# Kernel tuning notes

Hardware: AMD Instinct MI355X
Metric: run time of the kernel (lower is better)

The kernel has to match this reference:

```python
import jax, jax.numpy as jnp
import numpy as np

N_MEMORY = 16
FEA_DIM = 512


def setup_inputs() -> dict:
    key = jax.random.key(0)
    ks = jax.random.split(key, 8)
    b, L, d, n = 4, 4096, FEA_DIM, N_MEMORY
    scale = 1.0 / np.sqrt(d)  # ~ torch Linear default init scale
    return {
        "query": jax.random.normal(ks[0], (b, L, d), dtype=jnp.float32),
        "W1": jax.random.uniform(ks[1], (n, d, d), jnp.float32, -scale, scale),
        "b1": jax.random.uniform(ks[2], (n, d), jnp.float32, -scale, scale),
        "W2": jax.random.uniform(ks[3], (n, d, d), jnp.float32, -scale, scale),
        "b2": jax.random.uniform(ks[4], (n, d), jnp.float32, -scale, scale),
        "Wg": jax.random.uniform(ks[5], (n, d), jnp.float32, -scale, scale),
        "bg": jax.random.uniform(ks[6], (n,), jnp.float32, -scale, scale),
        "topk": 8,
    }


def reference(query, W1, b1, W2, b2, Wg, bg, topk):
    # query: [b, L, d]; stacked per-memory-slot params: W1/W2 [n, d, d], Wg [n, d]
    n = W1.shape[0]
    # per-slot LeakyReLU negative slopes: 0.01 + 0.2/n * l
    slopes = (0.01 + 0.2 / n * jnp.arange(n, dtype=query.dtype))[:, None, None, None]
    # memory_function: Linear -> LeakyReLU(slope_l) -> Linear -> Tanh, all slots at once
    h = jnp.einsum('bld,ndh->nblh', query, W1) + b1[:, None, None, :]   # [n,b,L,d]
    h = jnp.where(h >= 0, h, h * slopes)
    x = jnp.tanh(jnp.einsum('nblh,nhd->nbld', h, W2) + b2[:, None, None, :])  # [n,b,L,d]
    # gate: Linear(d,1) -> softmax over L -> topk over L -> gather -> weighted sum
    logits = jnp.einsum('nbld,nd->nbl', x, Wg) + bg[:, None, None]      # [n,b,L]
    w = jax.nn.softmax(logits, axis=-1)
    top_w, top_idx = jax.lax.top_k(w, topk)                             # [n,b,k]
    items = jnp.take_along_axis(x, top_idx[..., None], axis=2)          # [n,b,k,d]
    combined = jnp.einsum('nbkd,nbk->nbd', items, top_w)                # [n,b,d]
    m_item = jnp.transpose(combined, (1, 0, 2))                         # [b,n,d]
    # F.normalize(dim=-1), eps=1e-12
    norm = jnp.maximum(jnp.linalg.norm(m_item, axis=-1, keepdims=True), 1e-12)
    return m_item / norm
```

## Files before the change

kernel.cpp:

```cpp
#include <hip/hip_runtime.h>
#include <hip/hip_bf16.h>
#include <cstdint>
#include <cstddef>

#define NMEM 16
#define DDIM 512
#define BATCH 4
#define LSEQ 4096
#define ROWS 16384
#define NCAND 32
#define KTOP 8
#define QPAD 20

typedef __attribute__((ext_vector_type(4))) float f32x4;
typedef __attribute__((ext_vector_type(16))) float f32x16;
typedef __attribute__((ext_vector_type(8))) int int8v;

__device__ inline void gld16(const void* gptr, void* lptr) {
    __builtin_amdgcn_global_load_lds(
        (const __attribute__((address_space(1))) unsigned int*)gptr,
        (__attribute__((address_space(3))) unsigned int*)lptr,
        16, 0, 0);
}

__device__ inline float fast_tanh(float x) {
    float t = __builtin_amdgcn_fmed3f(x, -3.f, 3.f);
    float t2 = t * t;
    return t * (27.f + t2) * __builtin_amdgcn_rcpf(27.f + 9.f * t2);
}

__device__ inline int8v ldg_frag(const unsigned char* p) {
    int4 x = *(const int4*)p;
    int4 y = *(const int4*)(p + 16);
    int8v v;
    v[0] = x.x; v[1] = x.y; v[2] = x.z; v[3] = x.w;
    v[4] = y.x; v[5] = y.y; v[6] = y.z; v[7] = y.w;
    return v;
}

__device__ inline int8v load_frag_half(const unsigned char* Ts, int row, int kh) {
    int key = (row >> 1) & 3;
    const int4* p0 = (const int4*)(Ts + row * 64 + ((((kh << 1) | 0) ^ key) << 4));
    const int4* p1 = (const int4*)(Ts + row * 64 + ((((kh << 1) | 1) ^ key) << 4));
    int4 x = *p0, y = *p1;
    int8v v;
    v[0] = x.x; v[1] = x.y; v[2] = x.z; v[3] = x.w;
    v[4] = y.x; v[5] = y.y; v[6] = y.z; v[7] = y.w;
    return v;
}

__device__ inline void stage_half(const unsigned char* Wbase, unsigned char* dst,
                                  int tid) {
    #pragma unroll
    for (int i = 0; i < 2; ++i) {
        int c = i * 256 + tid;
        int row = c >> 2, s = c & 3;
        gld16(Wbase + (size_t)row * DDIM + ((s ^ ((row >> 1) & 3)) << 4),
              dst + c * 16);
    }
}

__global__ __launch_bounds__(256)
void prep_kernel(const float* __restrict__ query,
                 const float* __restrict__ W1, const float* __restrict__ W2,
                 unsigned char* __restrict__ Q8,
                 unsigned char* __restrict__ W1T8, unsigned char* __restrict__ W2T8) {
    int blk = blockIdx.x, t = threadIdx.x;
    if (blk < 2048) {
        size_t base = ((size_t)blk * 256 + t) * 16;
        const float4* in = (const float4*)(query + base);
        int4 o; int* op = (int*)&o;
        #pragma unroll
        for (int q = 0; q < 4; ++q) {
            float4 v = in[q];
            int lo = __builtin_amdgcn_cvt_pk_fp8_f32(v.x, v.y, 0, false);
            op[q] = __builtin_amdgcn_cvt_pk_fp8_f32(v.z, v.w, lo, true);
        }
        *(int4*)(Q8 + base) = o;
    } else {
        __shared__ float tile[64][69];
        int bid = blk - 2048;
        const float* Win = W1; unsigned char* Wout = W1T8;
        if (bid >= 1024) { bid -= 1024; Win = W2; Wout = W2T8; }
        int n = bid >> 6, t64 = bid & 63;
        int dt = (t64 >> 3) << 6, jt = (t64 & 7) << 6;
        const float* inN = Win + (size_t)n * DDIM * DDIM;
        unsigned char* outN = Wout + (size_t)n * DDIM * DDIM;
        int rr = t >> 4, cc = (t & 15) * 4;
        #pragma unroll
        for (int pass = 0; pass < 4; ++pass) {
            int row = rr + pass * 16;
            float4 v = *(const float4*)(inN + (size_t)(dt + row) * DDIM + jt + cc);
            tile[row][cc] = v.x; tile[row][cc + 1] = v.y;
            tile[row][cc + 2] = v.z; tile[row][cc + 3] = v.w;
        }
        __syncthreads();
        #pragma unroll
        for (int pass = 0; pass < 4; ++pass) {
            int jl = rr + pass * 16;
            float f0 = tile[cc][jl], f1 = tile[cc + 1][jl];
            float f2 = tile[cc + 2][jl], f3 = tile[cc + 3][jl];
            int lo = __builtin_amdgcn_cvt_pk_fp8_f32(f0, f1, 0, false);
            int dw = __builtin_amdgcn_cvt_pk_fp8_f32(f2, f3, lo, true);
            *(int*)(outN + (size_t)(jt + jl) * DDIM + dt + cc) = dw;
        }
    }
}

__global__ __launch_bounds__(256, 4)
void fused_mlp_kernel(const unsigned char* __restrict__ Q8,
                      const unsigned char* __restrict__ W1T8,
                      const unsigned char* __restrict__ W2T8,
                      const float* __restrict__ b1, const float* __restrict__ b2,
                      const float* __restrict__ Wg,
                      float* __restrict__ logits)
{
    __shared__ unsigned char hbuf[32 * 512];
    __shared__ unsigned char Bs[2][8192];
    __shared__ float lsum[4][32];
    const int id = blockIdx.x;
    const int n = id & 15;
    const int m0 = (id >> 4) * 32;
    const int tid = threadIdx.x, lane = tid & 63;
    const int w = tid >> 6;
    const int l31 = lane & 31, kh = lane >> 5;
    const unsigned char* W1n = W1T8 + (size_t)n * DDIM * DDIM;
    const unsigned char* W2n = W2T8 + (size_t)n * DDIM * DDIM;
    const float slope = 0.01f + 0.0125f * n;
    const unsigned char* Aq0 = Q8 + (size_t)(m0 + l31) * DDIM + kh * 32;

    int8v avq[8];
    #pragma unroll
    for (int qa = 0; qa < 8; ++qa)
        avq[qa] = ldg_frag(Aq0 + qa * 64);
    stage_half(W1n, Bs[0], tid);
    __syncthreads();

    #pragma unroll 1
    for (int n0 = 0; n0 < 4; ++n0) {
        f32x16 acc = {};
        #pragma unroll
        for (int p8 = 0; p8 < 8; ++p8) {
            const int P = n0 * 8 + p8, Pn = P + 1;
            const unsigned char* nsrc = (Pn < 32)
                ? W1n + (size_t)((Pn >> 3) * 128) * DDIM + (Pn & 7) * 64
                : W2n;
            stage_half(nsrc, Bs[Pn & 1], tid);
            const unsigned char* Ts = Bs[P & 1];
            int8v wfr = load_frag_half(Ts, w * 32 + l31, kh);
            acc = __builtin_amdgcn_mfma_scale_f32_32x32x64_f8f6f4(
                wfr, avq[p8], acc, 0, 0, 0, 0x7F7F7F7F, 0, 0x7F7F7F7F);
            __syncthreads();
        }
        {
            int r = l31;
            #pragma unroll
            for (int q = 0; q < 4; ++q) {
                int jb = n0 * 128 + w * 32 + 8 * q + 4 * kh;
                float4 bias = *(const float4*)(b1 + n * DDIM + jb);
                float v0 = acc[4 * q + 0] + bias.x;
                float v1 = acc[4 * q + 1] + bias.y;
                float v2 = acc[4 * q + 2] + bias.z;
                float v3 = acc[4 * q + 3] + bias.w;
                v0 = v0 >= 0.f ? v0 : v0 * slope;
                v1 = v1 >= 0.f ? v1 : v1 * slope;
                v2 = v2 >= 0.f ? v2 : v2 * slope;
                v3 = v3 >= 0.f ? v3 : v3 * slope;
                int lo = __builtin_amdgcn_cvt_pk_fp8_f32(v0, v1, 0, false);
                int dw = __builtin_amdgcn_cvt_pk_fp8_f32(v2, v3, lo, true);
                *(int*)(hbuf + r * 512 + ((((jb >> 4) ^ (r & 7)) << 4) | (jb & 15))) = dw;
            }
        }
    }

    __syncthreads();

    float rowacc[16] = {};
    #pragma unroll 1
    for (int n0 = 0; n0 < 4; ++n0) {
        f32x16 acc = {};
        #pragma unroll 1
        for (int p8 = 0; p8 < 8; ++p8) {
            const int P = 32 + n0 * 8 + p8, Pn = P + 1;
            if (Pn < 64)
                stage_half(W2n + (size_t)(((Pn - 32) >> 3) * 128) * DDIM
                               + ((Pn - 32) & 7) * 64,
                           Bs[Pn & 1], tid);
            int hrow = l31, hq = hrow & 7;
            int C0 = p8 * 4 + 2 * kh;
            int8v hv;
            {
                const int4* p0 = (const int4*)(hbuf + hrow * 512 + ((C0 ^ hq) << 4));
                const int4* p1 = (const int4*)(hbuf + hrow * 512 + (((C0 + 1) ^ hq) << 4));
                int4 x = *p0, y = *p1;
                hv[0] = x.x; hv[1] = x.y; hv[2] = x.z; hv[3] = x.w;
                hv[4] = y.x; hv[5] = y.y; hv[6] = y.z; hv[7] = y.w;
            }
            const unsigned char* Ts = Bs[P & 1];
            int8v wfr = load_frag_half(Ts, w * 32 + l31, kh);
            acc = __builtin_amdgcn_mfma_scale_f32_32x32x64_f8f6f4(
                hv, wfr, acc, 0, 0, 0, 0x7F7F7F7F, 0, 0x7F7F7F7F);
            __syncthreads();
        }
        {
            int j = n0 * 128 + w * 32 + l31;
            float bias = b2[n * DDIM + j];
            float wgv = Wg[n * DDIM + j];
            #pragma unroll
            for (int reg = 0; reg < 16; ++reg)
                rowacc[reg] = fmaf(fast_tanh(acc[reg] + bias), wgv, rowacc[reg]);
        }
    }
    #pragma unroll
    for (int sh = 1; sh < 32; sh <<= 1)
        #pragma unroll
        for (int reg = 0; reg < 16; ++reg)
            rowacc[reg] += __shfl_xor(rowacc[reg], sh);
    if (l31 == 0) {
        #pragma unroll
        for (int reg = 0; reg < 16; ++reg)
            lsum[w][(reg & 3) + 8 * (reg >> 2) + 4 * kh] = rowacc[reg];
    }
    __syncthreads();
    if (tid < 32)
        logits[(size_t)n * ROWS + m0 + tid] =
            lsum[0][tid] + lsum[1][tid] + lsum[2][tid] + lsum[3][tid];
}

__global__ __launch_bounds__(256)
void topcand_kernel(const float* __restrict__ logits, int* __restrict__ cand,
                    float* __restrict__ ex_logit) {
    __shared__ float lv[LSEQ];
    __shared__ float cv[128];
    __shared__ int   ci[128];
    int p = blockIdx.x, n = p >> 2, b = p & 3;
    int t = threadIdx.x, lane = t & 63, w = t >> 6;
    const float* L = logits + (size_t)n * ROWS + (size_t)b * LSEQ;
    for (int i = t; i < LSEQ; i += 256) lv[i] = L[i];
    __syncthreads();
    float mv[16];
    int base = w * 1024;
    #pragma unroll
    for (int j = 0; j < 16; ++j) mv[j] = lv[base + j * 64 + lane];
    for (int rd = 0; rd < 32; ++rd) {
        float best = mv[0]; int bj = 0;
        #pragma unroll
        for (int j = 1; j < 16; ++j)
            if (mv[j] > best) { best = mv[j]; bj = j; }
        int bidx = base + bj * 64 + lane;
        float rv = best; int ridx = bidx;
        #pragma unroll
        for (int s = 1; s < 64; s <<= 1) {
            float ov = __shfl_xor(rv, s); int oi = __shfl_xor(ridx, s);
            if (ov > rv || (ov == rv && oi < ridx)) { rv = ov; ridx = oi; }
        }
        if (lane == 0) { cv[w * 32 + rd] = rv; ci[w * 32 + rd] = ridx; }
        if (ridx == bidx) mv[bj] = -1e30f;
    }
    __syncthreads();
    if (w == 0) {
        float v2[2]; int i2[2];
        #pragma unroll
        for (int k = 0; k < 2; ++k) { v2[k] = cv[k * 64 + lane]; i2[k] = ci[k * 64 + lane]; }
        for (int rd = 0; rd < 32; ++rd) {
            float best = v2[0]; int bi = i2[0]; int bk = 0;
            if (v2[1] > best || (v2[1] == best && i2[1] < bi)) { best = v2[1]; bi = i2[1]; bk = 1; }
            float rv = best; int ridx = bi;
            #pragma unroll
            for (int s = 1; s < 64; s <<= 1) {
                float ov = __shfl_xor(rv, s); int oi = __shfl_xor(ridx, s);
                if (ov > rv || (ov == rv && oi < ridx)) { rv = ov; ridx = oi; }
            }
            if (lane == 0) cand[p * NCAND + rd] = ridx;
            if (ridx == bi) v2[bk] = -1e30f;
        }
    } else if (w == 1) {
        if (lane < NCAND) ex_logit[p * NCAND + lane] = 0.f;
    }
}

__global__ __launch_bounds__(256)
void exact_h_kernel(const float* __restrict__ query,
                    const float* __restrict__ W1, const float* __restrict__ b1,
                    const int* __restrict__ cand, float* __restrict__ ex_h) {
    __shared__ float qs[DDIM][QPAD];
    __shared__ float hpart[4][16][64];
    int blk = blockIdx.x;
    int p = blk >> 4, r4 = blk & 15;
    int ct = r4 >> 3, jc = r4 & 7;
    int n = p >> 2, b = p & 3;
    int t = threadIdx.x, jj = t & 63, dg = t >> 6;
    int j = jc * 64 + jj;
    for (int c = 0; c < 16; ++c) {
        int li = cand[p * NCAND + ct * 16 + c];
        const float* qr = query + ((size_t)b * LSEQ + li) * DDIM;
        for (int d = t; d < DDIM; d += 256) qs[d][c] = qr[d];
    }
    __syncthreads();
    const float* W1n = W1 + (size_t)n * DDIM * DDIM;
    float acc[16] = {};
    for (int d = dg * 128; d < dg * 128 + 128; ++d) {
        float wvv = W1n[(size_t)d * DDIM + j];
        const float4* qv = (const float4*)&qs[d][0];
        #pragma unroll
        for (int c4 = 0; c4 < 4; ++c4) {
            float4 q4 = qv[c4];
            acc[c4 * 4 + 0] = fmaf(q4.x, wvv, acc[c4 * 4 + 0]);
            acc[c4 * 4 + 1] = fmaf(q4.y, wvv, acc[c4 * 4 + 1]);
            acc[c4 * 4 + 2] = fmaf(q4.z, wvv, acc[c4 * 4 + 2]);
            acc[c4 * 4 + 3] = fmaf(q4.w, wvv, acc[c4 * 4 + 3]);
        }
    }
    #pragma unroll
    for (int c = 0; c < 16; ++c) hpart[dg][c][jj] = acc[c];
    __syncthreads();
    const float slope = 0.01f + 0.0125f * n;
    float bias = b1[n * DDIM + j];
    for (int cc = dg; cc < 16; cc += 4) {
        float h = hpart[0][cc][jj] + hpart[1][cc][jj] + hpart[2][cc][jj]
                + hpart[3][cc][jj] + bias;
        h = h >= 0.f ? h : h * slope;
        ex_h[((size_t)p * NCAND + ct * 16 + cc) * DDIM + j] = h;
    }
}

__global__ __launch_bounds__(256)
void exact_x_kernel(const float* __restrict__ ex_h,
                    const float* __restrict__ W2, const float* __restrict__ b2,
                    const float* __restrict__ Wg,
                    float* __restrict__ ex_x, float* __restrict__ ex_logit) {
    __shared__ float hs[DDIM][QPAD];
    __shared__ float xpart[4][16][64];
    int blk = blockIdx.x;
    int p = blk >> 4, r4 = blk & 15;
    int ct = r4 >> 3, jc = r4 & 7;
    int n = p >> 2;
    int t = threadIdx.x, jj = t & 63, dg = t >> 6;
    int j = jc * 64 + jj;
    for (int c = 0; c < 16; ++c) {
        const float* hr = ex_h + ((size_t)p * NCAND + ct * 16 + c) * DDIM;
        for (int d = t; d < DDIM; d += 256) hs[d][c] = hr[d];
    }
    __syncthreads();
    const float* W2n = W2 + (size_t)n * DDIM * DDIM;
    float acc[16] = {};
    for (int d = dg * 128; d < dg * 128 + 128; ++d) {
        float wvv = W2n[(size_t)d * DDIM + j];
        const float4* hv = (const float4*)&hs[d][0];
        #pragma unroll
        for (int c4 = 0; c4 < 4; ++c4) {
            float4 h4 = hv[c4];
            acc[c4 * 4 + 0] = fmaf(h4.x, wvv, acc[c4 * 4 + 0]);
            acc[c4 * 4 + 1] = fmaf(h4.y, wvv, acc[c4 * 4 + 1]);
            acc[c4 * 4 + 2] = fmaf(h4.z, wvv, acc[c4 * 4 + 2]);
            acc[c4 * 4 + 3] = fmaf(h4.w, wvv, acc[c4 * 4 + 3]);
        }
    }
    #pragma unroll
    for (int c = 0; c < 16; ++c) xpart[dg][c][jj] = acc[c];
    __syncthreads();
    float bias = b2[n * DDIM + j];
    float wg = Wg[n * DDIM + j];
    for (int cc = dg; cc < 16; cc += 4) {
        float a = xpart[0][cc][jj] + xpart[1][cc][jj] + xpart[2][cc][jj]
                + xpart[3][cc][jj] + bias;
        float x = tanhf(a);
        ex_x[((size_t)p * NCAND + ct * 16 + cc) * DDIM + j] = x;
        float lp = x * wg;
        #pragma unroll
        for (int s = 1; s < 64; s <<= 1) lp += __shfl_xor(lp, s);
        if (jj == 0) atomicAdd(&ex_logit[p * NCAND + ct * 16 + cc], lp);
    }
}

__global__ __launch_bounds__(64)
void final_kernel(const float* __restrict__ ex_x, const float* __restrict__ ex_logit,
                  const int* __restrict__ cand, float* __restrict__ out)
{
    __shared__ float w8s[KTOP];
    __shared__ int   s8s[KTOP];
    int p = blockIdx.x, n = p >> 2, b = p & 3;
    int t = threadIdx.x;
    float myv = (t < NCAND) ? ex_logit[p * NCAND + t] : -1e30f;
    int myidx = (t < NCAND) ? cand[p * NCAND + t] : 0x7fffffff;
    float lmax = 0.f;
    for (int k = 0; k < KTOP; ++k) {
        float rv = myv; int ridx = myidx; int rl = t;
        #pragma unroll
        for (int s = 1; s < 64; s <<= 1) {
            float ov = __shfl_xor(rv, s); int oi = __shfl_xor(ridx, s); int ol = __shfl_xor(rl, s);
            if (ov > rv || (ov == rv && oi < ridx)) { rv = ov; ridx = oi; rl = ol; }
        }
        if (k == 0) lmax = rv;
        if (t == 0) { w8s[k] = __expf(rv - lmax); s8s[k] = rl; }
        if (t == rl) myv = -1e30f;
    }
    __syncthreads();
    float cvv[8];
    float sq = 0.f;
    int idx = 0;
    for (int d = t; d < DDIM; d += 64, ++idx) {
        float s = 0.f;
        #pragma unroll
        for (int k = 0; k < KTOP; ++k)
            s = fmaf(w8s[k], ex_x[((size_t)p * NCAND + s8s[k]) * DDIM + d], s);
        cvv[idx] = s;
        sq += s * s;
    }
    #pragma unroll
    for (int s = 1; s < 64; s <<= 1) sq += __shfl_xor(sq, s);
    float norm = fmaxf(sqrtf(sq), 1e-12f);
    idx = 0;
    for (int d = t; d < DDIM; d += 64, ++idx)
        out[((size_t)b * NMEM + n) * DDIM + d] = cvv[idx] / norm;
}

extern "C" void kernel_launch(void* const* d_in, const int* in_sizes, int n_in,
                              void* d_out, int out_size, void* d_ws, size_t ws_size,
                              hipStream_t stream)
{
    const float* query = (const float*)d_in[0];
    const float* W1    = (const float*)d_in[1];
    const float* b1    = (const float*)d_in[2];
    const float* W2    = (const float*)d_in[3];
    const float* b2    = (const float*)d_in[4];
    const float* Wg    = (const float*)d_in[5];

    char* ws = (char*)d_ws;
    const size_t MB = 1024 * 1024;
    unsigned char* Q8   = (unsigned char*)(ws);
    unsigned char* W1T8 = (unsigned char*)(ws + 8 * MB);
    unsigned char* W2T8 = (unsigned char*)(ws + 12 * MB);
    float* logits   = (float*)(ws + 16 * MB);
    int*   cand     = (int*)  (ws + 17 * MB);
    float* ex_logit = (float*)(ws + 17 * MB + 16384);
    float* ex_h     = (float*)(ws + 20 * MB);
    float* ex_x     = (float*)(ws + 28 * MB);

    prep_kernel<<<4096, 256, 0, stream>>>(query, W1, W2, Q8, W1T8, W2T8);
    fused_mlp_kernel<<<8192, 256, 0, stream>>>(Q8, W1T8, W2T8, b1, b2, Wg, logits);
    topcand_kernel<<<64, 256, 0, stream>>>(logits, cand, ex_logit);
    exact_h_kernel<<<1024, 256, 0, stream>>>(query, W1, b1, cand, ex_h);
    exact_x_kernel<<<1024, 256, 0, stream>>>(ex_h, W2, b2, Wg, ex_x, ex_logit);
    final_kernel<<<64, 64, 0, stream>>>(ex_x, ex_logit, cand, (float*)d_out);
}
```

Before: 572.5 us.

## Process 64 rows per block with 2x2 wave layout and quarter weight tiles

```diff
diff --git a/kernel.cpp b/kernel.cpp
--- a/kernel.cpp
+++ b/kernel.cpp
@@ -38,7 +38,7 @@
     return v;
 }
 
-__device__ inline int8v load_frag_half(const unsigned char* Ts, int row, int kh) {
+__device__ inline int8v load_frag_q(const unsigned char* Ts, int row, int kh) {
     int key = (row >> 1) & 3;
     const int4* p0 = (const int4*)(Ts + row * 64 + ((((kh << 1) | 0) ^ key) << 4));
     const int4* p1 = (const int4*)(Ts + row * 64 + ((((kh << 1) | 1) ^ key) << 4));
@@ -49,15 +49,11 @@
     return v;
 }
 
-__device__ inline void stage_half(const unsigned char* Wbase, unsigned char* dst,
-                                  int tid) {
-    #pragma unroll
-    for (int i = 0; i < 2; ++i) {
-        int c = i * 256 + tid;
-        int row = c >> 2, s = c & 3;
-        gld16(Wbase + (size_t)row * DDIM + ((s ^ ((row >> 1) & 3)) << 4),
-              dst + c * 16);
-    }
+__device__ inline void stage_quarter(const unsigned char* Wbase,
+                                     unsigned char* dst, int tid) {
+    int row = tid >> 2, s = tid & 3;
+    gld16(Wbase + (size_t)row * DDIM + ((s ^ ((row >> 1) & 3)) << 4),
+          dst + tid * 16);
 }
 
 __global__ __launch_bounds__(256)
@@ -107,7 +103,7 @@
     }
 }
 
-__global__ __launch_bounds__(256, 4)
+__global__ __launch_bounds__(256, 2)
 void fused_mlp_kernel(const unsigned char* __restrict__ Q8,
                       const unsigned char* __restrict__ W1T8,
                       const unsigned char* __restrict__ W2T8,
@@ -115,48 +111,48 @@
                       const float* __restrict__ Wg,
                       float* __restrict__ logits)
 {
-    __shared__ unsigned char hbuf[32 * 512];
-    __shared__ unsigned char Bs[2][8192];
-    __shared__ float lsum[4][32];
+    __shared__ unsigned char hbuf[64 * 512];
+    __shared__ unsigned char Bs[2][4096];
     const int id = blockIdx.x;
     const int n = id & 15;
-    const int m0 = (id >> 4) * 32;
+    const int m0 = (id >> 4) * 64;
     const int tid = threadIdx.x, lane = tid & 63;
     const int w = tid >> 6;
+    const int rh = w >> 1, ch = w & 1;
     const int l31 = lane & 31, kh = lane >> 5;
     const unsigned char* W1n = W1T8 + (size_t)n * DDIM * DDIM;
     const unsigned char* W2n = W2T8 + (size_t)n * DDIM * DDIM;
     const float slope = 0.01f + 0.0125f * n;
-    const unsigned char* Aq0 = Q8 + (size_t)(m0 + l31) * DDIM + kh * 32;
+    const unsigned char* Aq0 = Q8 + (size_t)(m0 + rh * 32 + l31) * DDIM + kh * 32;
 
     int8v avq[8];
     #pragma unroll
     for (int qa = 0; qa < 8; ++qa)
         avq[qa] = ldg_frag(Aq0 + qa * 64);
-    stage_half(W1n, Bs[0], tid);
+    stage_quarter(W1n, Bs[0], tid);
     __syncthreads();
 
     #pragma unroll 1
-    for (int n0 = 0; n0 < 4; ++n0) {
+    for (int c8 = 0; c8 < 8; ++c8) {
         f32x16 acc = {};
         #pragma unroll
         for (int p8 = 0; p8 < 8; ++p8) {
-            const int P = n0 * 8 + p8, Pn = P + 1;
-            const unsigned char* nsrc = (Pn < 32)
-                ? W1n + (size_t)((Pn >> 3) * 128) * DDIM + (Pn & 7) * 64
+            const int P = c8 * 8 + p8, Pn = P + 1;
+            const unsigned char* nsrc = (Pn < 64)
+                ? W1n + (size_t)((Pn >> 3) * 64) * DDIM + (Pn & 7) * 64
                 : W2n;
-            stage_half(nsrc, Bs[Pn & 1], tid);
+            stage_quarter(nsrc, Bs[Pn & 1], tid);
             const unsigned char* Ts = Bs[P & 1];
-            int8v wfr = load_frag_half(Ts, w * 32 + l31, kh);
+            int8v wfr = load_frag_q(Ts, ch * 32 + l31, kh);
             acc = __builtin_amdgcn_mfma_scale_f32_32x32x64_f8f6f4(
                 wfr, avq[p8], acc, 0, 0, 0, 0x7F7F7F7F, 0, 0x7F7F7F7F);
             __syncthreads();
         }
         {
-            int r = l31;
+            int r = rh * 32 + l31;
             #pragma unroll
             for (int q = 0; q < 4; ++q) {
-                int jb = n0 * 128 + w * 32 + 8 * q + 4 * kh;
+                int jb = c8 * 64 + ch * 32 + 8 * q + 4 * kh;
                 float4 bias = *(const float4*)(b1 + n * DDIM + jb);
                 float v0 = acc[4 * q + 0] + bias.x;
                 float v1 = acc[4 * q + 1] + bias.y;
@@ -177,16 +173,16 @@
 
     float rowacc[16] = {};
     #pragma unroll 1
-    for (int n0 = 0; n0 < 4; ++n0) {
+    for (int c8 = 0; c8 < 8; ++c8) {
         f32x16 acc = {};
         #pragma unroll 1
         for (int p8 = 0; p8 < 8; ++p8) {
-            const int P = 32 + n0 * 8 + p8, Pn = P + 1;
-            if (Pn < 64)
-                stage_half(W2n + (size_t)(((Pn - 32) >> 3) * 128) * DDIM
-                               + ((Pn - 32) & 7) * 64,
-                           Bs[Pn & 1], tid);
-            int hrow = l31, hq = hrow & 7;
+            const int P = 64 + c8 * 8 + p8, Pn = P + 1;
+            if (Pn < 128)
+                stage_quarter(W2n + (size_t)(((Pn - 64) >> 3) * 64) * DDIM
+                                  + ((Pn - 64) & 7) * 64,
+                              Bs[Pn & 1], tid);
+            int hrow = rh * 32 + l31, hq = hrow & 7;
             int C0 = p8 * 4 + 2 * kh;
             int8v hv;
             {
@@ -197,13 +193,13 @@
                 hv[4] = y.x; hv[5] = y.y; hv[6] = y.z; hv[7] = y.w;
             }
             const unsigned char* Ts = Bs[P & 1];
-            int8v wfr = load_frag_half(Ts, w * 32 + l31, kh);
+            int8v wfr = load_frag_q(Ts, ch * 32 + l31, kh);
             acc = __builtin_amdgcn_mfma_scale_f32_32x32x64_f8f6f4(
                 hv, wfr, acc, 0, 0, 0, 0x7F7F7F7F, 0, 0x7F7F7F7F);
             __syncthreads();
         }
         {
-            int j = n0 * 128 + w * 32 + l31;
+            int j = c8 * 64 + ch * 32 + l31;
             float bias = b2[n * DDIM + j];
             float wgv = Wg[n * DDIM + j];
             #pragma unroll
@@ -216,15 +212,17 @@
         #pragma unroll
         for (int reg = 0; reg < 16; ++reg)
             rowacc[reg] += __shfl_xor(rowacc[reg], sh);
+    __syncthreads();
+    float* lsum = (float*)hbuf;
     if (l31 == 0) {
         #pragma unroll
         for (int reg = 0; reg < 16; ++reg)
-            lsum[w][(reg & 3) + 8 * (reg >> 2) + 4 * kh] = rowacc[reg];
-    }
-    __syncthreads();
-    if (tid < 32)
-        logits[(size_t)n * ROWS + m0 + tid] =
-            lsum[0][tid] + lsum[1][tid] + lsum[2][tid] + lsum[3][tid];
+            lsum[ch * 64 + rh * 32 + (reg & 3) + 8 * (reg >> 2) + 4 * kh]
+                = rowacc[reg];
+    }
+    __syncthreads();
+    if (tid < 64)
+        logits[(size_t)n * ROWS + m0 + tid] = lsum[tid] + lsum[64 + tid];
 }
 
 __global__ __launch_bounds__(256)
@@ -438,7 +436,7 @@
     float* ex_x     = (float*)(ws + 28 * MB);
 
     prep_kernel<<<4096, 256, 0, stream>>>(query, W1, W2, Q8, W1T8, W2T8);
-    fused_mlp_kernel<<<8192, 256, 0, stream>>>(Q8, W1T8, W2T8, b1, b2, Wg, logits);
+    fused_mlp_kernel<<<4096, 256, 0, stream>>>(Q8, W1T8, W2T8, b1, b2, Wg, logits);
     topcand_kernel<<<64, 256, 0, stream>>>(logits, cand, ex_logit);
     exact_h_kernel<<<1024, 256, 0, stream>>>(query, W1, b1, cand, ex_h);
     exact_x_kernel<<<1024, 256, 0, stream>>>(ex_h, W2, b2, Wg, ex_x, ex_logit);
```

Result: faster. 464.1 us (-18.9%).
